# Kernel tuning notes

Measured on AMD Instinct MI355X. Metric: run time of the kernel, lower is better.

The kernel has to match this reference:

```python
import jax, jax.numpy as jnp
import numpy as np

T_LEN, S_LEN, B = 100, 400, 16
D_IN, H, CTX, V = 512, 512, 1024, 50000


def setup_inputs() -> dict:
    key = jax.random.key(0)
    ks = jax.random.split(key, 16)
    p = lambda k, shp: jax.random.normal(k, shp, dtype=jnp.float32) * 0.05
    return {
        "y_emb": p(ks[0], (T_LEN, B, D_IN)),
        "context": p(ks[1], (S_LEN, B, CTX)),
        "init_h": p(ks[2], (B, H)),
        "init_c": p(ks[3], (B, H)),
        "x_mask": jnp.ones((S_LEN, B, 1), jnp.float32),
        "y_mask": jnp.ones((T_LEN, B, 1), jnp.float32),
        "y_idx": jax.random.randint(ks[4], (T_LEN, B), 0, V),
        # LSTMCell params (PyTorch gate order i,f,g,o)
        "W_ih": p(ks[5], (4 * H, D_IN)),
        "W_hh": p(ks[6], (4 * H, H)),
        "b_ih": jnp.zeros((4 * H,), jnp.float32),
        "b_hh": jnp.zeros((4 * H,), jnp.float32),
        # second gate block (order i,f,o,c per chunk names x4i,x4f,x4o,x4c)
        "Wx": p(ks[7], (4 * H, CTX)),
        "Ux": p(ks[8], (4 * H, H)),
        "bx": jnp.zeros((4 * H,), jnp.float32),
        # attention params
        "Wc_att": p(ks[9], (CTX, CTX)),
        "b_att": jnp.zeros((CTX,), jnp.float32),
        "W_comb_att": p(ks[10], (CTX, 2 * H)),
        "U_att": p(ks[11], (1, CTX)),
        # word prob: softmax(Linear(cat[h2, att, y_emb]))
        "Wp": p(ks[12], (V, H + CTX + D_IN)),
        "bp": jnp.zeros((V,), jnp.float32),
    }


def reference(y_emb, context, init_h, init_c, x_mask, y_mask, y_idx,
              W_ih, W_hh, b_ih, b_hh, Wx, Ux, bx,
              Wc_att, b_att, W_comb_att, U_att, Wp, bp):
    # pctx: [S, B, CTX]
    pctx = jnp.einsum('sbc,dc->sbd', context, Wc_att) + b_att
    u_att = U_att[0]  # [CTX]

    def step(carry, inp):
        h, c = carry              # [B, H] each
        y, ym, yi = inp           # [B, D_IN], [B, 1], [B]
        # LSTMCell (gate order i, f, g, o)
        gates = y @ W_ih.T + b_ih + h @ W_hh.T + b_hh
        gi, gf, gg, go = jnp.split(gates, 4, axis=1)
        c1 = jax.nn.sigmoid(gf) * c + jax.nn.sigmoid(gi) * jnp.tanh(gg)
        h1 = jax.nn.sigmoid(go) * jnp.tanh(c1)
        h1 = ym * h1 + (1.0 - ym) * h
        c1 = ym * c1 + (1.0 - ym) * c
        # attention query from cat(h1, c1)
        s = jnp.concatenate([h1, c1], axis=1)          # [B, 2H]
        q = s @ W_comb_att.T                           # [B, CTX]
        unreg = jnp.tanh(pctx + q) * x_mask            # [S, B, CTX]
        u = jnp.einsum('sbc,c->sb', unreg, u_att)[..., None]  # [S, B, 1]
        w = jnp.exp(u - jnp.max(u, axis=0, keepdims=True)) * x_mask
        w = w / jnp.sum(w, axis=0, keepdims=True)      # [S, B, 1]
        att = jnp.sum(w * context, axis=0)             # [B, CTX]
        # second gate block (chunk order i, f, o, c)
        pre = h1 @ Ux.T + att @ Wx.T + bx
        xi, xf, xo, xc = jnp.split(pre, 4, axis=1)
        c2 = jax.nn.sigmoid(xf) * c1 + jax.nn.sigmoid(xi) * jnp.tanh(xc)
        h2 = jax.nn.sigmoid(xo) * jnp.tanh(c2)
        c2 = ym * c2 + (1.0 - ym) * c1
        h2 = ym * h2 + (1.0 - ym) * h1
        # word prob + per-step NLL
        feat = jnp.concatenate([h2, att, y], axis=1)   # [B, H+CTX+D_IN]
        logp = jax.nn.log_softmax(feat @ Wp.T + bp, axis=1)
        cost = -jnp.take_along_axis(logp, yi[:, None], axis=1)[:, 0]  # [B]
        return (h2, c2), cost

    _, costs = jax.lax.scan(step, (init_h, init_c), (y_emb, y_mask, y_idx))
    ym2 = y_mask[..., 0]                               # [T, B]
    cost_per_batch = jnp.sum(costs * ym2, axis=0) / jnp.sum(ym2, axis=0)
    return cost_per_batch
```

## Files before the change

kernel.cpp:

```cpp
#include <hip/hip_runtime.h>
#include <stdint.h>

typedef unsigned int u32;
typedef unsigned short u16;
typedef unsigned char u8;
typedef long long i64;
typedef __attribute__((ext_vector_type(4))) float f32x4;
typedef __attribute__((ext_vector_type(4))) float f32x4v;
typedef __attribute__((ext_vector_type(8))) short bf16x8;

#define T_LEN 100
#define S_LEN 400
#define NB 16
#define HD 512
#define CTXD 1024
#define VOC 50000
#define K4H 2048
#define M_ALL 1600

static __device__ __forceinline__ float bf2f(u16 v) {
  union { u32 u; float f; } c; c.u = ((u32)v) << 16; return c.f;
}
static __device__ __forceinline__ u16 f2bf(float f) {
  union { float f; u32 u; } c; c.f = f;
  return (u16)((c.u + 0x7fffu + ((c.u >> 16) & 1u)) >> 16);
}
static __device__ __forceinline__ u32 pack2(float a, float b) {
  return (u32)f2bf(a) | ((u32)f2bf(b) << 16);
}
static __device__ __forceinline__ uint4 pack8(float4 a, float4 b) {
  return make_uint4(pack2(a.x, a.y), pack2(a.z, a.w), pack2(b.x, b.y), pack2(b.z, b.w));
}
static __device__ __forceinline__ uint4 pack8v(f32x4v a, f32x4v b) {
  return make_uint4(pack2(a.x, a.y), pack2(a.z, a.w), pack2(b.x, b.y), pack2(b.z, b.w));
}
static __device__ __forceinline__ u32 pkfp8(float x, float y, float z, float w) {
  int p = 0;
  p = __builtin_amdgcn_cvt_pk_fp8_f32(x, y, p, 0);
  p = __builtin_amdgcn_cvt_pk_fp8_f32(z, w, p, 1);
  return (u32)p;
}
static __device__ __forceinline__ float sigm(float x) { return 1.f / (1.f + __expf(-x)); }
static __device__ __forceinline__ float tanh_(float x) {
  float e = __expf(2.f * x);
  return 1.f - 2.f / (e + 1.f);
}
static __device__ __forceinline__ float ald(const float* p) {
  return __hip_atomic_load(p, __ATOMIC_RELAXED, __HIP_MEMORY_SCOPE_AGENT);
}
static __device__ __forceinline__ void ast(float* p, float v) {
  __hip_atomic_store(p, v, __ATOMIC_RELAXED, __HIP_MEMORY_SCOPE_AGENT);
}
static __device__ __forceinline__ f32x4v cld4(const float* p) {
  f32x4v v;
  asm volatile("global_load_dwordx4 %0, %1, off sc0 sc1\n\t"
               "s_waitcnt vmcnt(0)"
               : "=&v"(v) : "v"(p) : "memory");
  return v;
}
static __device__ __forceinline__ void cld8(
    const float* p0, const float* p1, const float* p2, const float* p3,
    const float* p4, const float* p5, const float* p6, const float* p7,
    f32x4v& v0, f32x4v& v1, f32x4v& v2, f32x4v& v3,
    f32x4v& v4, f32x4v& v5, f32x4v& v6, f32x4v& v7) {
  asm volatile(
      "global_load_dwordx4 %0, %8, off sc0 sc1\n\t"
      "global_load_dwordx4 %1, %9, off sc0 sc1\n\t"
      "global_load_dwordx4 %2, %10, off sc0 sc1\n\t"
      "global_load_dwordx4 %3, %11, off sc0 sc1\n\t"
      "global_load_dwordx4 %4, %12, off sc0 sc1\n\t"
      "global_load_dwordx4 %5, %13, off sc0 sc1\n\t"
      "global_load_dwordx4 %6, %14, off sc0 sc1\n\t"
      "global_load_dwordx4 %7, %15, off sc0 sc1\n\t"
      "s_waitcnt vmcnt(0)"
      : "=&v"(v0), "=&v"(v1), "=&v"(v2), "=&v"(v3),
        "=&v"(v4), "=&v"(v5), "=&v"(v6), "=&v"(v7)
      : "v"(p0), "v"(p1), "v"(p2), "v"(p3), "v"(p4), "v"(p5), "v"(p6), "v"(p7)
      : "memory");
}

__global__ void sentinel_kernel(float* out, float v) {
  if (threadIdx.x < NB) out[threadIdx.x] = v;
}

struct CastArgs {
  const float* src[9];
  u16* dst[9];
  u32 cum[10];
};

__global__ __launch_bounds__(256) void cast_all(CastArgs A) {
  u32 i = blockIdx.x * 256 + threadIdx.x;
  if (i >= A.cum[9]) return;
  int seg = 0;
  while (i >= A.cum[seg + 1]) seg++;
  u32 li = i - A.cum[seg];
  const float* s = A.src[seg];
  f32x4v a = __builtin_nontemporal_load((const f32x4v*)&s[li * 8]);
  f32x4v b = __builtin_nontemporal_load((const f32x4v*)&s[li * 8 + 4]);
  if (seg < 8) {
    *(uint4*)&A.dst[seg][li * 8] = pack8v(a, b);
  } else {
    u32 m = li >> 6, k8 = (li & 63) << 3;
    u8* f8 = (u8*)A.dst[8];
    uint2 t;
    t.x = pkfp8(a.x, a.y, a.z, a.w);
    t.y = pkfp8(b.x, b.y, b.z, b.w);
    *(uint2*)&f8[(size_t)m * K4H + 1536 + k8] = t;
  }
}

template <int MODE>
__global__ __launch_bounds__(256) void gemm_bf16(const u16* __restrict__ A,
                                                 const u16* __restrict__ Bw,
                                                 void* __restrict__ out,
                                                 const float* __restrict__ bias1,
                                                 const float* __restrict__ bias2,
                                                 int M, int N, int K) {
  __shared__ u16 As[64][40];
  __shared__ u16 Bs[64][40];
  int nb = N / 64;
  int m0 = (blockIdx.x / nb) * 64;
  int n0 = (blockIdx.x % nb) * 64;
  int tid = threadIdx.x;
  int lane = tid & 63;
  int w = tid >> 6;
  int wm = (w >> 1) * 32, wn = (w & 1) * 32;
  f32x4 acc[2][2] = {};
  int arow = tid >> 2, achk = (tid & 3) * 8;
  for (int k0 = 0; k0 < K; k0 += 32) {
    __syncthreads();
    *(uint4*)&As[arow][achk] = *(const uint4*)&A[(size_t)(m0 + arow) * K + k0 + achk];
    *(uint4*)&Bs[arow][achk] = *(const uint4*)&Bw[(size_t)(n0 + arow) * K + k0 + achk];
    __syncthreads();
    int r = lane & 15, kg = lane >> 4;
    bf16x8 a0 = *(const bf16x8*)&As[wm + r][kg * 8];
    bf16x8 a1 = *(const bf16x8*)&As[wm + 16 + r][kg * 8];
    bf16x8 b0 = *(const bf16x8*)&Bs[wn + r][kg * 8];
    bf16x8 b1 = *(const bf16x8*)&Bs[wn + 16 + r][kg * 8];
    acc[0][0] = __builtin_amdgcn_mfma_f32_16x16x32_bf16(a0, b0, acc[0][0], 0, 0, 0);
    acc[0][1] = __builtin_amdgcn_mfma_f32_16x16x32_bf16(a0, b1, acc[0][1], 0, 0, 0);
    acc[1][0] = __builtin_amdgcn_mfma_f32_16x16x32_bf16(a1, b0, acc[1][0], 0, 0, 0);
    acc[1][1] = __builtin_amdgcn_mfma_f32_16x16x32_bf16(a1, b1, acc[1][1], 0, 0, 0);
  }
  int col = lane & 15, rg = lane >> 4;
#pragma unroll
  for (int fi = 0; fi < 2; fi++)
#pragma unroll
    for (int fj = 0; fj < 2; fj++)
#pragma unroll
      for (int r = 0; r < 4; r++) {
        int m = m0 + wm + fi * 16 + rg * 4 + r;
        int n = n0 + wn + fj * 16 + col;
        float v = acc[fi][fj][r] + bias1[n];
        if constexpr (MODE == 1) {
          v += bias2[n];
          ((float*)out)[(size_t)m * N + n] = v;
        } else {
          ((u16*)out)[(size_t)m * N + n] = f2bf(v);
        }
      }
}

struct DecArgs {
  const u16 *pctx, *ctx, *Whh, *Wcomb, *Uxw, *Wxw;
  const float *xW, *bx, *uatt, *xmask, *ymask, *init_h, *init_c;
  float *h, *c, *h1, *c1, *qsum, *attnum, *attden;
  u8* feat8;
  u32* bar;
};

static __device__ __forceinline__ void gbar(u32* bar, u32 gen) {
  __syncthreads();
  if (threadIdx.x == 0) {
    asm volatile("s_waitcnt vmcnt(0) lgkmcnt(0)" ::: "memory");
    const int g = blockIdx.x >> 4;
    u32* gcnt = bar + 1088 + g * 64;
    u32* gflag = bar + 64 + g * 64;
    u32 old = __hip_atomic_fetch_add(gcnt, 1u, __ATOMIC_RELAXED, __HIP_MEMORY_SCOPE_AGENT);
    if (old == gen * 16u - 1u) {
      u32 r = __hip_atomic_fetch_add(bar, 1u, __ATOMIC_RELAXED, __HIP_MEMORY_SCOPE_AGENT);
      if (r == gen * 16u - 1u) {
        for (int i = 0; i < 16; i++)
          __hip_atomic_store(bar + 64 + i * 64, gen, __ATOMIC_RELAXED,
                             __HIP_MEMORY_SCOPE_AGENT);
      }
    }
    while (__hip_atomic_load(gflag, __ATOMIC_RELAXED, __HIP_MEMORY_SCOPE_AGENT) < gen)
      __builtin_amdgcn_s_sleep(4);
    asm volatile("" ::: "memory");
  }
  __syncthreads();
}

__global__ __launch_bounds__(256, 1) void decoder_coop(DecArgs A) {
  extern __shared__ char smem[];
  u16* pctx_l = (u16*)smem;
  u16* ctx_l = (u16*)(smem + 51200);
  float* ua_lp = (float*)(smem + 102400);
  float* xm_l = (float*)(smem + 106752);
  char* un = smem + 106880;

  const int tid = threadIdx.x;
  const int blk = blockIdx.x;
  const int lane = tid & 63, w = tid >> 6;
  const int r16 = lane & 15, kg = lane >> 4;
  const int bK = blk & 15;
  const int s0 = (blk >> 4) * 25;
  u32 gen = 1;

  for (int idx = tid; idx < 25 * 128; idx += 256) {
    int i = idx >> 7, c8 = (idx & 127) << 3;
    *(uint4*)&pctx_l[i * 1024 + c8] =
        *(const uint4*)&A.pctx[((size_t)(s0 + i) * NB + bK) * CTXD + c8];
    *(uint4*)&ctx_l[i * 1024 + c8] =
        *(const uint4*)&A.ctx[((size_t)(s0 + i) * NB + bK) * CTXD + c8];
  }
  {
    int c0 = tid * 4;
    int p = (c0 >> 4) * 17 + (c0 & 15);
#pragma unroll
    for (int j = 0; j < 4; j++) ua_lp[p + j] = A.uatt[c0 + j];
  }
  if (tid < 25) xm_l[tid] = A.xmask[(s0 + tid) * NB + bK];

  for (int ts = 0; ts < T_LEN; ts++) {
    const int par = ts & 1;
    if (blk < 16) {
      u16* Al = (u16*)un;
      float* gbA = (float*)(un + 16640);
      u16* h1c1 = (u16*)(un + 24832);
      const float* hs = ts ? A.h : A.init_h;
      const float* cs = ts ? A.c : A.init_c;
      {
        const int b0_ = tid >> 6, k80 = (tid & 63) << 3;
        const int b1_ = (256 + tid) >> 6, k81 = ((256 + tid) & 63) << 3;
        const int b2_ = (512 + tid) >> 6, k82 = ((512 + tid) & 63) << 3;
        const int b3_ = (768 + tid) >> 6, k83 = ((768 + tid) & 63) << 3;
        f32x4v v0, v1, v2, v3, v4, v5, v6, v7;
        cld8(&hs[b0_ * 512 + k80], &hs[b0_ * 512 + k80 + 4],
             &hs[b1_ * 512 + k81], &hs[b1_ * 512 + k81 + 4],
             &hs[b2_ * 512 + k82], &hs[b2_ * 512 + k82 + 4],
             &hs[b3_ * 512 + k83], &hs[b3_ * 512 + k83 + 4],
             v0, v1, v2, v3, v4, v5, v6, v7);
        *(uint4*)&Al[b0_ * 520 + k80] = pack8v(v0, v1);
        *(uint4*)&Al[b1_ * 520 + k81] = pack8v(v2, v3);
        *(uint4*)&Al[b2_ * 520 + k82] = pack8v(v4, v5);
        *(uint4*)&Al[b3_ * 520 + k83] = pack8v(v6, v7);
      }
      __syncthreads();
      const int j0 = blk * 32;
      {
        f32x4 acc0 = {}, acc1 = {};
        const size_t row0 = (size_t)(w * 512 + j0 + r16) * 512;
        const size_t row1 = (size_t)(w * 512 + j0 + 16 + r16) * 512;
#pragma unroll
        for (int ks = 0; ks < 16; ks++) {
          bf16x8 a = *(const bf16x8*)&Al[r16 * 520 + ks * 32 + kg * 8];
          bf16x8 b0 = *(const bf16x8*)&A.Whh[row0 + ks * 32 + kg * 8];
          bf16x8 b1 = *(const bf16x8*)&A.Whh[row1 + ks * 32 + kg * 8];
          acc0 = __builtin_amdgcn_mfma_f32_16x16x32_bf16(a, b0, acc0, 0, 0, 0);
          acc1 = __builtin_amdgcn_mfma_f32_16x16x32_bf16(a, b1, acc1, 0, 0, 0);
        }
#pragma unroll
        for (int r = 0; r < 4; r++) {
          gbA[(w * 16 + kg * 4 + r) * 32 + r16] = acc0[r];
          gbA[(w * 16 + kg * 4 + r) * 32 + 16 + r16] = acc1[r];
        }
      }
      __syncthreads();
#pragma unroll
      for (int i = 0; i < 2; i++) {
        int idx = i * 256 + tid;
        int b = idx >> 5, j = idx & 31;
        int n = j0 + j;
        const float* xw = &A.xW[(size_t)(ts * NB + b) * K4H];
        float gi = gbA[(0 * 16 + b) * 32 + j] + xw[n];
        float gf = gbA[(1 * 16 + b) * 32 + j] + xw[512 + n];
        float gg = gbA[(2 * 16 + b) * 32 + j] + xw[1024 + n];
        float go = gbA[(3 * 16 + b) * 32 + j] + xw[1536 + n];
        float ymv = A.ymask[ts * NB + b];
        float c_old = ald(&cs[b * 512 + n]);
        float h_old = ald(&hs[b * 512 + n]);
        float c1v = sigm(gf) * c_old + sigm(gi) * tanh_(gg);
        float h1v = sigm(go) * tanh_(c1v);
        h1v = ymv * h1v + (1.f - ymv) * h_old;
        c1v = ymv * c1v + (1.f - ymv) * c_old;
        ast(&A.h1[b * 512 + n], h1v);
        ast(&A.c1[b * 512 + n], c1v);
        h1c1[b * 72 + j] = f2bf(h1v);
        h1c1[b * 72 + 32 + j] = f2bf(c1v);
      }
      __syncthreads();
      {
        bf16x8 a0 = *(const bf16x8*)&h1c1[r16 * 72 + kg * 8];
        bf16x8 a1 = *(const bf16x8*)&h1c1[r16 * 72 + 32 + kg * 8];
        float* qs = A.qsum + par * 16384;
        for (int nt = w; nt < 64; nt += 4) {
          int n = nt * 16 + r16;
          bf16x8 b0 = *(const bf16x8*)&A.Wcomb[(size_t)n * 1024 + j0 + kg * 8];
          bf16x8 b1 = *(const bf16x8*)&A.Wcomb[(size_t)n * 1024 + 512 + j0 + kg * 8];
          f32x4 acc = {};
          acc = __builtin_amdgcn_mfma_f32_16x16x32_bf16(a0, b0, acc, 0, 0, 0);
          acc = __builtin_amdgcn_mfma_f32_16x16x32_bf16(a1, b1, acc, 0, 0, 0);
#pragma unroll
          for (int r = 0; r < 4; r++)
            atomicAdd(&qs[(kg * 4 + r) * 1024 + nt * 16 + r16], acc[r]);
        }
      }
    }
    gbar(A.bar, gen); gen++;
    {
      float* q_lp = (float*)un;
      float* p_l = (float*)(un + 4352);
      {
        int c0 = tid * 4;
        f32x4v qv = cld4(&A.qsum[par * 16384 + bK * 1024 + c0]);
        int p = (c0 >> 4) * 17 + (c0 & 15);
        q_lp[p] = qv.x; q_lp[p + 1] = qv.y; q_lp[p + 2] = qv.z; q_lp[p + 3] = qv.w;
      }
      __syncthreads();
      for (int i = w; i < 25; i += 4) {
        const u16* prow = &pctx_l[i * 1024 + lane * 16];
        float s = 0.f;
#pragma unroll
        for (int half = 0; half < 2; half++) {
          bf16x8 pv = *(const bf16x8*)&prow[half * 8];
#pragma unroll
          for (int e = 0; e < 8; e++) {
            int cc = lane * 17 + half * 8 + e;
            s += tanh_(bf2f((u16)pv[e]) + q_lp[cc]) * ua_lp[cc];
          }
        }
#pragma unroll
        for (int off = 1; off < 64; off <<= 1) s += __shfl_xor(s, off);
        if (lane == 0) {
          float xm = xm_l[i];
          p_l[i] = __expf(s * xm) * xm;
        }
      }
      __syncthreads();
      const int c4 = tid << 2;
      float n0 = 0, n1 = 0, n2 = 0, n3 = 0;
#pragma unroll 5
      for (int i = 0; i < 25; i++) {
        float pv = p_l[i];
        uint2 ld = *(const uint2*)&ctx_l[i * 1024 + c4];
        n0 += pv * bf2f((u16)(ld.x & 0xffff));
        n1 += pv * bf2f((u16)(ld.x >> 16));
        n2 += pv * bf2f((u16)(ld.y & 0xffff));
        n3 += pv * bf2f((u16)(ld.y >> 16));
      }
      float* dst = &A.attnum[par * 16384 + bK * 1024 + c4];
      atomicAdd(dst + 0, n0);
      atomicAdd(dst + 1, n1);
      atomicAdd(dst + 2, n2);
      atomicAdd(dst + 3, n3);
      if (tid == 0) {
        float d = 0.f;
        for (int i = 0; i < 25; i++) d += p_l[i];
        atomicAdd(&A.attden[par * NB + bK], d);
      }
    }
    gbar(A.bar, gen); gen++;
    if (blk < 32) {
      u16* AlD = (u16*)un;
      float* gbD = (float*)(un + 49408);
      float* attden_l = (float*)(un + 53504);
      if (tid < NB) attden_l[tid] = ald(&A.attden[par * NB + tid]);
      {
        const int b0_ = tid >> 6, k80 = (tid & 63) << 3;
        const int b1_ = (256 + tid) >> 6, k81 = ((256 + tid) & 63) << 3;
        const int b2_ = (512 + tid) >> 6, k82 = ((512 + tid) & 63) << 3;
        const int b3_ = (768 + tid) >> 6, k83 = ((768 + tid) & 63) << 3;
        f32x4v v0, v1, v2, v3, v4, v5, v6, v7;
        cld8(&A.h1[b0_ * 512 + k80], &A.h1[b0_ * 512 + k80 + 4],
             &A.h1[b1_ * 512 + k81], &A.h1[b1_ * 512 + k81 + 4],
             &A.h1[b2_ * 512 + k82], &A.h1[b2_ * 512 + k82 + 4],
             &A.h1[b3_ * 512 + k83], &A.h1[b3_ * 512 + k83 + 4],
             v0, v1, v2, v3, v4, v5, v6, v7);
        *(uint4*)&AlD[b0_ * 1544 + k80] = pack8v(v0, v1);
        *(uint4*)&AlD[b1_ * 1544 + k81] = pack8v(v2, v3);
        *(uint4*)&AlD[b2_ * 1544 + k82] = pack8v(v4, v5);
        *(uint4*)&AlD[b3_ * 1544 + k83] = pack8v(v6, v7);
      }
      __syncthreads();
      {
        const float* base = &A.attnum[par * 16384];
        const int c4 = tid << 2;
        f32x4v a0, a1, a2, a3, a4, a5, a6, a7;
        cld8(base + 0 * 1024 + c4, base + 1 * 1024 + c4, base + 2 * 1024 + c4,
             base + 3 * 1024 + c4, base + 4 * 1024 + c4, base + 5 * 1024 + c4,
             base + 6 * 1024 + c4, base + 7 * 1024 + c4,
             a0, a1, a2, a3, a4, a5, a6, a7);
#define ATT_ST(i, vv)                                                        \
  {                                                                          \
    float rd = 1.f / attden_l[i];                                            \
    uint2 t;                                                                 \
    t.x = pack2(vv.x * rd, vv.y * rd);                                       \
    t.y = pack2(vv.z * rd, vv.w * rd);                                       \
    *(uint2*)&AlD[(i) * 1544 + 512 + c4] = t;                                \
  }
        ATT_ST(0, a0) ATT_ST(1, a1) ATT_ST(2, a2) ATT_ST(3, a3)
        ATT_ST(4, a4) ATT_ST(5, a5) ATT_ST(6, a6) ATT_ST(7, a7)
        cld8(base + 8 * 1024 + c4, base + 9 * 1024 + c4, base + 10 * 1024 + c4,
             base + 11 * 1024 + c4, base + 12 * 1024 + c4, base + 13 * 1024 + c4,
             base + 14 * 1024 + c4, base + 15 * 1024 + c4,
             a0, a1, a2, a3, a4, a5, a6, a7);
        ATT_ST(8, a0) ATT_ST(9, a1) ATT_ST(10, a2) ATT_ST(11, a3)
        ATT_ST(12, a4) ATT_ST(13, a5) ATT_ST(14, a6) ATT_ST(15, a7)
#undef ATT_ST
      }
      __syncthreads();
      if (blk < 16) {
        const u16* arow = &AlD[blk * 1544 + 512];
        int c4 = tid * 4;
        u32 p = pkfp8(bf2f(arow[c4]), bf2f(arow[c4 + 1]), bf2f(arow[c4 + 2]),
                      bf2f(arow[c4 + 3]));
        *(u32*)&A.feat8[(size_t)(ts * NB + blk) * K4H + 512 + c4] = p;
      }
      const int j0 = blk * 16;
      f32x4 acc = {};
      const size_t rowU = (size_t)(w * 512 + j0 + r16) * 512;
      const size_t rowW = (size_t)(w * 512 + j0 + r16) * 1024;
#pragma unroll
      for (int ks = 0; ks < 16; ks++) {
        bf16x8 a = *(const bf16x8*)&AlD[r16 * 1544 + ks * 32 + kg * 8];
        bf16x8 b0 = *(const bf16x8*)&A.Uxw[rowU + ks * 32 + kg * 8];
        acc = __builtin_amdgcn_mfma_f32_16x16x32_bf16(a, b0, acc, 0, 0, 0);
      }
#pragma unroll
      for (int ks = 16; ks < 48; ks++) {
        bf16x8 a = *(const bf16x8*)&AlD[r16 * 1544 + ks * 32 + kg * 8];
        bf16x8 b0 = *(const bf16x8*)&A.Wxw[rowW + (ks - 16) * 32 + kg * 8];
        acc = __builtin_amdgcn_mfma_f32_16x16x32_bf16(a, b0, acc, 0, 0, 0);
      }
#pragma unroll
      for (int r = 0; r < 4; r++) gbD[(w * 16 + kg * 4 + r) * 16 + r16] = acc[r];
      __syncthreads();
      {
        int b = tid >> 4, j = tid & 15;
        int n = j0 + j;
        float xi = gbD[(0 * 16 + b) * 16 + j] + A.bx[n];
        float xf = gbD[(1 * 16 + b) * 16 + j] + A.bx[512 + n];
        float xo = gbD[(2 * 16 + b) * 16 + j] + A.bx[1024 + n];
        float xc = gbD[(3 * 16 + b) * 16 + j] + A.bx[1536 + n];
        float ymv = A.ymask[ts * NB + b];
        float c1v = ald(&A.c1[b * 512 + n]);
        float h1v = ald(&A.h1[b * 512 + n]);
        float c2 = sigm(xf) * c1v + sigm(xi) * tanh_(xc);
        float h2 = sigm(xo) * tanh_(c2);
        c2 = ymv * c2 + (1.f - ymv) * c1v;
        h2 = ymv * h2 + (1.f - ymv) * h1v;
        ast(&A.h[b * 512 + n], h2);
        ast(&A.c[b * 512 + n], c2);
        int p8 = 0;
        p8 = __builtin_amdgcn_cvt_pk_fp8_f32(h2, h2, p8, 0);
        A.feat8[(size_t)(ts * NB + b) * K4H + n] = (u8)(p8 & 0xff);
      }
      ast(&A.attnum[(par ^ 1) * 16384 + blk * 512 + tid], 0.f);
      ast(&A.attnum[(par ^ 1) * 16384 + blk * 512 + 256 + tid], 0.f);
      ast(&A.qsum[par * 16384 + blk * 512 + tid], 0.f);
      ast(&A.qsum[par * 16384 + blk * 512 + 256 + tid], 0.f);
      if (blk == 0 && tid < NB) ast(&A.attden[(par ^ 1) * NB + tid], 0.f);
    }
    gbar(A.bar, gen); gen++;
  }
}

__global__ __launch_bounds__(512, 1) void lse_gemm_fp8(const u8* __restrict__ feat8,
                                                       const float* __restrict__ Wp,
                                                       const float* __restrict__ bp,
                                                       float* __restrict__ lse) {
  extern __shared__ char smem[];
  u8* Bl = (u8*)smem;
  const int tid = threadIdx.x;
  const int n0 = blockIdx.x * 64;
  for (int n = 0; n < 64; n++) {
    int gn = n0 + n;
    f32x4v f = {0.f, 0.f, 0.f, 0.f};
    if (gn < VOC)
      f = __builtin_nontemporal_load((const f32x4v*)&Wp[(size_t)gn * K4H + tid * 4]);
    *(u32*)&Bl[n * 2064 + tid * 4] = pkfp8(f.x, f.y, f.z, f.w);
  }
  __syncthreads();
  const int w = tid >> 6, lane = tid & 63;
  const int r16 = lane & 15, kg = lane >> 4;
  bool vj[4];
  float bpj[4];
#pragma unroll
  for (int j = 0; j < 4; j++) {
    int nf = n0 + j * 16 + r16;
    vj[j] = nf < VOC;
    bpj[j] = vj[j] ? bp[nf] : 0.f;
  }
  for (int qq = w; qq < 25; qq += 8) {
    int mrow = qq * 64;
    f32x4 acc[4][4] = {};
    for (int ks = 0; ks < 64; ks++) {
      i64 b0 = *(const i64*)&Bl[(r16) * 2064 + ks * 32 + kg * 8];
      i64 b1 = *(const i64*)&Bl[(16 + r16) * 2064 + ks * 32 + kg * 8];
      i64 b2 = *(const i64*)&Bl[(32 + r16) * 2064 + ks * 32 + kg * 8];
      i64 b3 = *(const i64*)&Bl[(48 + r16) * 2064 + ks * 32 + kg * 8];
#pragma unroll
      for (int s = 0; s < 4; s++) {
        i64 a = *(const i64*)&feat8[(size_t)(mrow + s * 16 + r16) * K4H + ks * 32 + kg * 8];
        acc[s][0] = __builtin_amdgcn_mfma_f32_16x16x32_fp8_fp8(a, b0, acc[s][0], 0, 0, 0);
        acc[s][1] = __builtin_amdgcn_mfma_f32_16x16x32_fp8_fp8(a, b1, acc[s][1], 0, 0, 0);
        acc[s][2] = __builtin_amdgcn_mfma_f32_16x16x32_fp8_fp8(a, b2, acc[s][2], 0, 0, 0);
        acc[s][3] = __builtin_amdgcn_mfma_f32_16x16x32_fp8_fp8(a, b3, acc[s][3], 0, 0, 0);
      }
    }
#pragma unroll
    for (int s = 0; s < 4; s++) {
#pragma unroll
      for (int r = 0; r < 4; r++) {
        float e = 0.f;
#pragma unroll
        for (int j = 0; j < 4; j++)
          if (vj[j]) e += __expf(acc[s][j][r] + bpj[j]);
        e += __shfl_xor(e, 1);
        e += __shfl_xor(e, 2);
        e += __shfl_xor(e, 4);
        e += __shfl_xor(e, 8);
        if (r16 == 0) atomicAdd(&lse[mrow + s * 16 + kg * 4 + r], e);
      }
    }
  }
}

__global__ __launch_bounds__(256) void target_logit(const u8* __restrict__ feat8,
                                                    const float* __restrict__ Wp,
                                                    const float* __restrict__ bp,
                                                    const int* __restrict__ yidx,
                                                    float* __restrict__ tlog) {
  int gw = (blockIdx.x * 256 + threadIdx.x) >> 6;
  int lane = threadIdx.x & 63;
  if (gw >= M_ALL) return;
  int yi = yidx[gw];
  const float* wrow = Wp + (size_t)yi * K4H;
  const u8* frow = feat8 + (size_t)gw * K4H;
  float s = 0.f;
#pragma unroll
  for (int i = 0; i < 4; i++) {
    int k = i * 512 + lane * 8;
    uint2 fv = *(const uint2*)&frow[k];
    f32x4v w0 = __builtin_nontemporal_load((const f32x4v*)&wrow[k]);
    f32x4v w1 = __builtin_nontemporal_load((const f32x4v*)&wrow[k + 4]);
    s += __builtin_amdgcn_cvt_f32_fp8(fv.x, 0) * w0.x;
    s += __builtin_amdgcn_cvt_f32_fp8(fv.x, 1) * w0.y;
    s += __builtin_amdgcn_cvt_f32_fp8(fv.x, 2) * w0.z;
    s += __builtin_amdgcn_cvt_f32_fp8(fv.x, 3) * w0.w;
    s += __builtin_amdgcn_cvt_f32_fp8(fv.y, 0) * w1.x;
    s += __builtin_amdgcn_cvt_f32_fp8(fv.y, 1) * w1.y;
    s += __builtin_amdgcn_cvt_f32_fp8(fv.y, 2) * w1.z;
    s += __builtin_amdgcn_cvt_f32_fp8(fv.y, 3) * w1.w;
  }
#pragma unroll
  for (int off = 1; off < 64; off <<= 1) s += __shfl_xor(s, off);
  if (lane == 0) tlog[gw] = s + bp[yi];
}

__global__ void finalize(const float* __restrict__ lse, const float* __restrict__ tlog,
                         const float* __restrict__ ymask, float* __restrict__ out) {
  int b = threadIdx.x;
  if (b < NB) {
    float sc = 0.f, sm = 0.f;
    for (int t = 0; t < T_LEN; t++) {
      int m = t * NB + b;
      float ym = ymask[m];
      sc += (logf(lse[m]) - tlog[m]) * ym;
      sm += ym;
    }
    out[b] = sc / sm;
  }
}

extern "C" void kernel_launch(void* const* d_in, const int* in_sizes, int n_in,
                              void* d_out, int out_size, void* d_ws, size_t ws_size,
                              hipStream_t stream) {
  const float* y_emb = (const float*)d_in[0];
  const float* context = (const float*)d_in[1];
  const float* init_h = (const float*)d_in[2];
  const float* init_c = (const float*)d_in[3];
  const float* x_mask = (const float*)d_in[4];
  const float* y_mask = (const float*)d_in[5];
  const int* y_idx = (const int*)d_in[6];
  const float* W_ih = (const float*)d_in[7];
  const float* W_hh = (const float*)d_in[8];
  const float* b_ih = (const float*)d_in[9];
  const float* b_hh = (const float*)d_in[10];
  const float* Wx = (const float*)d_in[11];
  const float* Ux = (const float*)d_in[12];
  const float* bx = (const float*)d_in[13];
  const float* Wc_att = (const float*)d_in[14];
  const float* b_att = (const float*)d_in[15];
  const float* W_comb = (const float*)d_in[16];
  const float* U_att = (const float*)d_in[17];
  const float* Wp = (const float*)d_in[18];
  const float* bp = (const float*)d_in[19];

  if (ws_size < 60000000ULL) {
    sentinel_kernel<<<1, 64, 0, stream>>>((float*)d_out, (float)(ws_size >> 20));
    return;
  }

  char* ws = (char*)d_ws;
  float* lse = (float*)(ws + 0);
  float* attnum = (float*)(ws + 8192);
  float* attden = (float*)(ws + 139264);
  u32* bar = (u32*)(ws + 139392);
  float* qsum = (float*)(ws + 151680);
  float* tlog = (float*)(ws + 282752);
  u16* pctx = (u16*)(ws + 294912);
  u16* ctxb = (u16*)(ws + 13402112);
  u16* Wcb = (u16*)(ws + 26509312);
  u16* yembb = (u16*)(ws + 28606464);
  u16* Wihb = (u16*)(ws + 30244864);
  u16* Whhb = (u16*)(ws + 32342016);
  u16* Wcombb = (u16*)(ws + 34439168);
  u16* Uxb = (u16*)(ws + 36536320);
  u16* Wxb = (u16*)(ws + 38633472);
  float* xW = (float*)(ws + 42827776);
  u8* feat8 = (u8*)(ws + 55934976);
  float* hbuf = (float*)(ws + 59211776);
  float* cbuf = (float*)(ws + 59244544);
  float* h1buf = (float*)(ws + 59277312);
  float* c1buf = (float*)(ws + 59310080);

  hipMemsetAsync(ws, 0, 282752, stream);

  CastArgs ca;
  ca.src[0] = context;  ca.dst[0] = ctxb;
  ca.src[1] = Wc_att;   ca.dst[1] = Wcb;
  ca.src[2] = y_emb;    ca.dst[2] = yembb;
  ca.src[3] = W_ih;     ca.dst[3] = Wihb;
  ca.src[4] = W_hh;     ca.dst[4] = Whhb;
  ca.src[5] = W_comb;   ca.dst[5] = Wcombb;
  ca.src[6] = Ux;       ca.dst[6] = Uxb;
  ca.src[7] = Wx;       ca.dst[7] = Wxb;
  ca.src[8] = y_emb;    ca.dst[8] = (u16*)feat8;
  u32 sz[9] = {819200, 131072, 102400, 131072, 131072, 131072, 131072, 262144, 102400};
  ca.cum[0] = 0;
  for (int i = 0; i < 9; i++) ca.cum[i + 1] = ca.cum[i] + sz[i];
  cast_all<<<(ca.cum[9] + 255) / 256, 256, 0, stream>>>(ca);

  gemm_bf16<0><<<1600, 256, 0, stream>>>(ctxb, Wcb, pctx, b_att, b_att, 6400, 1024, 1024);
  gemm_bf16<1><<<800, 256, 0, stream>>>(yembb, Wihb, xW, b_ih, b_hh, 1600, 2048, 512);

  DecArgs a;
  a.pctx = pctx; a.ctx = ctxb; a.Whh = Whhb; a.Wcomb = Wcombb; a.Uxw = Uxb; a.Wxw = Wxb;
  a.xW = xW; a.bx = bx; a.uatt = U_att; a.xmask = x_mask; a.ymask = y_mask;
  a.init_h = init_h; a.init_c = init_c;
  a.h = hbuf; a.c = cbuf; a.h1 = h1buf; a.c1 = c1buf; a.qsum = qsum;
  a.attnum = attnum; a.attden = attden; a.feat8 = feat8; a.bar = bar;
  hipFuncSetAttribute(reinterpret_cast<const void*>(decoder_coop),
                      hipFuncAttributeMaxDynamicSharedMemorySize, 160448);
  decoder_coop<<<256, 256, 160448, stream>>>(a);

  hipFuncSetAttribute(reinterpret_cast<const void*>(lse_gemm_fp8),
                      hipFuncAttributeMaxDynamicSharedMemorySize, 132096);
  lse_gemm_fp8<<<782, 512, 132096, stream>>>(feat8, Wp, bp, lse);

  target_logit<<<400, 256, 0, stream>>>(feat8, Wp, bp, y_idx, tlog);
  finalize<<<1, 64, 0, stream>>>(lse, tlog, y_mask, (float*)d_out);
}
```

Before: 5.136 ms.

## Replace grid-wide barriers with per-stage producer/consumer counters

Removes the three hierarchical grid barriers per timestep in the persistent decoder kernel. In their place are monotonic counters: each stage signals completion, and only the blocks that consume its output spin until the counter reaches the expected count. Blocks outside a stage no longer wait for it, and the spin sleep is shortened, which cuts synchronisation latency on the sequential recurrence. The risk is memory ordering: the signal is a relaxed atomic without the explicit vmcnt wait the old barrier issued, so ordering relative to earlier atomics and stores is weaker.

```diff
diff --git a/kernel.cpp b/kernel.cpp
--- a/kernel.cpp
+++ b/kernel.cpp
@@ -77,6 +77,13 @@
         "=&v"(v4), "=&v"(v5), "=&v"(v6), "=&v"(v7)
       : "v"(p0), "v"(p1), "v"(p2), "v"(p3), "v"(p4), "v"(p5), "v"(p6), "v"(p7)
       : "memory");
+}
+static __device__ __forceinline__ void sig(u32* ctr) {
+  __hip_atomic_fetch_add(ctr, 1u, __ATOMIC_RELAXED, __HIP_MEMORY_SCOPE_AGENT);
+}
+static __device__ __forceinline__ void waitge(u32* ctr, u32 tgt) {
+  while (__hip_atomic_load(ctr, __ATOMIC_RELAXED, __HIP_MEMORY_SCOPE_AGENT) < tgt)
+    __builtin_amdgcn_s_sleep(1);
 }
 
 __global__ void sentinel_kernel(float* out, float v) {
@@ -170,29 +177,6 @@
   u32* bar;
 };
 
-static __device__ __forceinline__ void gbar(u32* bar, u32 gen) {
-  __syncthreads();
-  if (threadIdx.x == 0) {
-    asm volatile("s_waitcnt vmcnt(0) lgkmcnt(0)" ::: "memory");
-    const int g = blockIdx.x >> 4;
-    u32* gcnt = bar + 1088 + g * 64;
-    u32* gflag = bar + 64 + g * 64;
-    u32 old = __hip_atomic_fetch_add(gcnt, 1u, __ATOMIC_RELAXED, __HIP_MEMORY_SCOPE_AGENT);
-    if (old == gen * 16u - 1u) {
-      u32 r = __hip_atomic_fetch_add(bar, 1u, __ATOMIC_RELAXED, __HIP_MEMORY_SCOPE_AGENT);
-      if (r == gen * 16u - 1u) {
-        for (int i = 0; i < 16; i++)
-          __hip_atomic_store(bar + 64 + i * 64, gen, __ATOMIC_RELAXED,
-                             __HIP_MEMORY_SCOPE_AGENT);
-      }
-    }
-    while (__hip_atomic_load(gflag, __ATOMIC_RELAXED, __HIP_MEMORY_SCOPE_AGENT) < gen)
-      __builtin_amdgcn_s_sleep(4);
-    asm volatile("" ::: "memory");
-  }
-  __syncthreads();
-}
-
 __global__ __launch_bounds__(256, 1) void decoder_coop(DecArgs A) {
   extern __shared__ char smem[];
   u16* pctx_l = (u16*)smem;
@@ -207,7 +191,9 @@
   const int r16 = lane & 15, kg = lane >> 4;
   const int bK = blk & 15;
   const int s0 = (blk >> 4) * 25;
-  u32 gen = 1;
+  u32* qdone = A.bar;
+  u32* cdone = A.bar + 64;
+  u32* h2done = A.bar + 128;
 
   for (int idx = tid; idx < 25 * 128; idx += 256) {
     int i = idx >> 7, c8 = (idx & 127) << 3;
@@ -227,6 +213,8 @@
   for (int ts = 0; ts < T_LEN; ts++) {
     const int par = ts & 1;
     if (blk < 16) {
+      if (tid == 0) waitge(h2done, 32u * (u32)ts);
+      __syncthreads();
       u16* Al = (u16*)un;
       float* gbA = (float*)(un + 16640);
       u16* h1c1 = (u16*)(un + 24832);
@@ -308,9 +296,12 @@
             atomicAdd(&qs[(kg * 4 + r) * 1024 + nt * 16 + r16], acc[r]);
         }
       }
+      __syncthreads();
+      if (tid == 0) sig(qdone);
     }
-    gbar(A.bar, gen); gen++;
     {
+      if (tid == 0) waitge(qdone, 16u * (u32)(ts + 1));
+      __syncthreads();
       float* q_lp = (float*)un;
       float* p_l = (float*)(un + 4352);
       {
@@ -361,9 +352,12 @@
         for (int i = 0; i < 25; i++) d += p_l[i];
         atomicAdd(&A.attden[par * NB + bK], d);
       }
+      __syncthreads();
+      if (tid == 0) sig(cdone);
     }
-    gbar(A.bar, gen); gen++;
     if (blk < 32) {
+      if (tid == 0) waitge(cdone, 256u * (u32)(ts + 1));
+      __syncthreads();
       u16* AlD = (u16*)un;
       float* gbD = (float*)(un + 49408);
       float* attden_l = (float*)(un + 53504);
@@ -463,8 +457,9 @@
       ast(&A.qsum[par * 16384 + blk * 512 + tid], 0.f);
       ast(&A.qsum[par * 16384 + blk * 512 + 256 + tid], 0.f);
       if (blk == 0 && tid < NB) ast(&A.attden[(par ^ 1) * NB + tid], 0.f);
+      __syncthreads();
+      if (tid == 0) sig(h2done);
     }
-    gbar(A.bar, gen); gen++;
   }
 }
 
```

Measured after the change: 5.052 ms. No clear change (-1.6%).
